# Optimization experiments

Hardware: AMD Instinct MI355X
Metric: run time of the kernel (lower is better)

The kernel has to match this reference:

```python
import jax, jax.numpy as jnp
import numpy as np

B, T, D = 8, 8192, 768

def setup_inputs() -> dict:
    key = jax.random.key(0)
    k1, k2 = jax.random.split(key)
    x = jax.random.normal(k1, (B, T, D), dtype=jnp.float32)
    stimulus = jax.random.normal(k2, (B, T, D), dtype=jnp.float32)
    return {"x": x, "stimulus": stimulus}

def reference(x, stimulus):
    # Per-position dot product: out[b, t] = sum_d x[b, t, d] * stimulus[b, t, d]
    return jnp.einsum("btd,btd->bt", x, stimulus)
```

## Files before the change

### kernel.cpp

```cpp
#include <hip/hip_runtime.h>


constexpr int D = 768;
constexpr int D4 = D / 4;
constexpr int ROWS = 8 * 8192;

__global__ __launch_bounds__(256) void row_dot_kernel(
    const float4* __restrict__ x,
    const float4* __restrict__ s,
    float* __restrict__ out)
{
    const int wave = (blockIdx.x * blockDim.x + threadIdx.x) >> 6;
    const int lane = threadIdx.x & 63;
    if (wave >= ROWS) return;

    const size_t base = (size_t)wave * D4;

    float acc = 0.0f;
#pragma unroll
    for (int c = 0; c < 3; ++c) {
        float4 a = x[base + c * 64 + lane];
        float4 b = s[base + c * 64 + lane];
        acc = fmaf(a.x, b.x, acc);
        acc = fmaf(a.y, b.y, acc);
        acc = fmaf(a.z, b.z, acc);
        acc = fmaf(a.w, b.w, acc);
    }

#pragma unroll
    for (int off = 32; off > 0; off >>= 1)
        acc += __shfl_down(acc, off, 64);

    if (lane == 0) out[wave] = acc;
}

extern "C" void kernel_launch(void* const* d_in, const int* in_sizes, int n_in,
                              void* d_out, int out_size, void* d_ws, size_t ws_size,
                              hipStream_t stream)
{
    const float4* x = (const float4*)d_in[0];
    const float4* s = (const float4*)d_in[1];
    float* out = (float*)d_out;

    const int waves_per_block = 4;
    const int blocks = ROWS / waves_per_block;
    row_dot_kernel<<<blocks, 256, 0, stream>>>(x, s, out);
}
```

Baseline: 380.9 us.

## Process eight rows per wavefront with batched loads and vectorized output stores

Each wavefront now handles eight consecutive rows instead of one, issuing all six float4 loads per row in an unrolled loop so many memory requests are in flight per wave. Reductions use xor shuffles, and lane 0 writes the eight results as two float4 stores. The grid shrinks eightfold and the launch bounds request higher occupancy. This costs more registers per thread and fewer waves overall, which could reduce latency hiding on a purely bandwidth-bound workload.

```diff
diff --git a/kernel.cpp b/kernel.cpp
--- a/kernel.cpp
+++ b/kernel.cpp
@@ -1,37 +1,61 @@
 #include <hip/hip_runtime.h>
 
 
-constexpr int D = 768;
-constexpr int D4 = D / 4;
+constexpr int D4   = 768 / 4;
 constexpr int ROWS = 8 * 8192;
+constexpr int RPW  = 8;
 
-__global__ __launch_bounds__(256) void row_dot_kernel(
+__global__ __launch_bounds__(256, 8) void row_dot_kernel(
     const float4* __restrict__ x,
     const float4* __restrict__ s,
-    float* __restrict__ out)
+    float4* __restrict__ out4)
 {
     const int wave = (blockIdx.x * blockDim.x + threadIdx.x) >> 6;
     const int lane = threadIdx.x & 63;
-    if (wave >= ROWS) return;
 
-    const size_t base = (size_t)wave * D4;
+    const size_t row0 = (size_t)wave * RPW;
 
-    float acc = 0.0f;
+    float acc[RPW];
 #pragma unroll
-    for (int c = 0; c < 3; ++c) {
-        float4 a = x[base + c * 64 + lane];
-        float4 b = s[base + c * 64 + lane];
-        acc = fmaf(a.x, b.x, acc);
-        acc = fmaf(a.y, b.y, acc);
-        acc = fmaf(a.z, b.z, acc);
-        acc = fmaf(a.w, b.w, acc);
+    for (int r = 0; r < RPW; ++r) {
+        const size_t base = (row0 + r) * D4 + lane;
+        float4 a0 = x[base];
+        float4 b0 = s[base];
+        float4 a1 = x[base + 64];
+        float4 b1 = s[base + 64];
+        float4 a2 = x[base + 128];
+        float4 b2 = s[base + 128];
+        float t = 0.0f;
+        t = fmaf(a0.x, b0.x, t);
+        t = fmaf(a0.y, b0.y, t);
+        t = fmaf(a0.z, b0.z, t);
+        t = fmaf(a0.w, b0.w, t);
+        t = fmaf(a1.x, b1.x, t);
+        t = fmaf(a1.y, b1.y, t);
+        t = fmaf(a1.z, b1.z, t);
+        t = fmaf(a1.w, b1.w, t);
+        t = fmaf(a2.x, b2.x, t);
+        t = fmaf(a2.y, b2.y, t);
+        t = fmaf(a2.z, b2.z, t);
+        t = fmaf(a2.w, b2.w, t);
+        acc[r] = t;
     }
 
 #pragma unroll
-    for (int off = 32; off > 0; off >>= 1)
-        acc += __shfl_down(acc, off, 64);
+    for (int r = 0; r < RPW; ++r) {
+        float v = acc[r];
+#pragma unroll
+        for (int off = 32; off > 0; off >>= 1)
+            v += __shfl_xor(v, off, 64);
+        acc[r] = v;
+    }
 
-    if (lane == 0) out[wave] = acc;
+    if (lane == 0) {
+        float4 o0 = make_float4(acc[0], acc[1], acc[2], acc[3]);
+        float4 o1 = make_float4(acc[4], acc[5], acc[6], acc[7]);
+        out4[(size_t)wave * 2]     = o0;
+        out4[(size_t)wave * 2 + 1] = o1;
+    }
 }
 
 extern "C" void kernel_launch(void* const* d_in, const int* in_sizes, int n_in,
@@ -40,9 +64,8 @@
 {
     const float4* x = (const float4*)d_in[0];
     const float4* s = (const float4*)d_in[1];
-    float* out = (float*)d_out;
+    float4* out4 = (float4*)d_out;
 
-    const int waves_per_block = 4;
-    const int blocks = ROWS / waves_per_block;
-    row_dot_kernel<<<blocks, 256, 0, stream>>>(x, s, out);
+    const int blocks = (ROWS / RPW) / 4;
+    row_dot_kernel<<<blocks, 256, 0, stream>>>(x, s, out4);
 }
```

Measured after the change: 388.0 us. No clear change (+1.9%).

## Process eight rows per wave with register double-buffered prefetch

Applied to the files above, without the earlier changes.

Each wavefront now handles eight consecutive rows instead of one, loading the next row's x and stimulus float4 chunks into registers while the current row is reduced. The grid shrinks eightfold and launch bounds request higher occupancy. The aim is to keep more memory requests in flight per wave and amortize launch and reduction overhead on a bandwidth-bound kernel. The cost is doubled register use for the prefetch buffers and fewer total waves to hide latency.

```diff
diff --git a/kernel.cpp b/kernel.cpp
--- a/kernel.cpp
+++ b/kernel.cpp
@@ -1,37 +1,59 @@
 #include <hip/hip_runtime.h>
 
 
-constexpr int D = 768;
-constexpr int D4 = D / 4;
+constexpr int D4   = 768 / 4;
 constexpr int ROWS = 8 * 8192;
+constexpr int RPW  = 8;
 
-__global__ __launch_bounds__(256) void row_dot_kernel(
+__global__ __launch_bounds__(256, 8) void row_dot_kernel(
     const float4* __restrict__ x,
     const float4* __restrict__ s,
     float* __restrict__ out)
 {
     const int wave = (blockIdx.x * blockDim.x + threadIdx.x) >> 6;
     const int lane = threadIdx.x & 63;
-    if (wave >= ROWS) return;
 
-    const size_t base = (size_t)wave * D4;
+    const size_t row0 = (size_t)wave * RPW;
+    size_t p = row0 * D4 + lane;
 
-    float acc = 0.0f;
-#pragma unroll
-    for (int c = 0; c < 3; ++c) {
-        float4 a = x[base + c * 64 + lane];
-        float4 b = s[base + c * 64 + lane];
-        acc = fmaf(a.x, b.x, acc);
-        acc = fmaf(a.y, b.y, acc);
-        acc = fmaf(a.z, b.z, acc);
-        acc = fmaf(a.w, b.w, acc);
-    }
+    float4 ca0 = x[p];       float4 cb0 = s[p];
+    float4 ca1 = x[p + 64];  float4 cb1 = s[p + 64];
+    float4 ca2 = x[p + 128]; float4 cb2 = s[p + 128];
 
 #pragma unroll
-    for (int off = 32; off > 0; off >>= 1)
-        acc += __shfl_down(acc, off, 64);
+    for (int r = 0; r < RPW; ++r) {
+        float4 na0, na1, na2, nb0, nb1, nb2;
+        if (r < RPW - 1) {
+            const size_t q = p + D4;
+            na0 = x[q];       nb0 = s[q];
+            na1 = x[q + 64];  nb1 = s[q + 64];
+            na2 = x[q + 128]; nb2 = s[q + 128];
+        }
 
-    if (lane == 0) out[wave] = acc;
+        float t = 0.0f;
+        t = fmaf(ca0.x, cb0.x, t);
+        t = fmaf(ca0.y, cb0.y, t);
+        t = fmaf(ca0.z, cb0.z, t);
+        t = fmaf(ca0.w, cb0.w, t);
+        t = fmaf(ca1.x, cb1.x, t);
+        t = fmaf(ca1.y, cb1.y, t);
+        t = fmaf(ca1.z, cb1.z, t);
+        t = fmaf(ca1.w, cb1.w, t);
+        t = fmaf(ca2.x, cb2.x, t);
+        t = fmaf(ca2.y, cb2.y, t);
+        t = fmaf(ca2.z, cb2.z, t);
+        t = fmaf(ca2.w, cb2.w, t);
+
+#pragma unroll
+        for (int off = 32; off > 0; off >>= 1)
+            t += __shfl_xor(t, off, 64);
+
+        if (lane == 0) out[row0 + r] = t;
+
+        p += D4;
+        ca0 = na0; ca1 = na1; ca2 = na2;
+        cb0 = nb0; cb1 = nb1; cb2 = nb2;
+    }
 }
 
 extern "C" void kernel_launch(void* const* d_in, const int* in_sizes, int n_in,
@@ -42,7 +64,6 @@
     const float4* s = (const float4*)d_in[1];
     float* out = (float*)d_out;
 
-    const int waves_per_block = 4;
-    const int blocks = ROWS / waves_per_block;
+    const int blocks = (ROWS / RPW) / 4;
     row_dot_kernel<<<blocks, 256, 0, stream>>>(x, s, out);
 }
```

After: 392.8 us. 1.03x slower.

## Process eight rows per wave with double-buffered register prefetch

Applied to the files above, without the earlier changes.

Each wave now handles eight rows, two at a time, issuing loads for the next pair before computing the current pair so more memory requests stay in flight. Reductions use xor shuffles for two rows at once, and sched_barrier keeps the compiler from reordering loads and math. This trades more registers and fewer total waves for higher per-wave memory-level parallelism and less launch and tail overhead.

```diff
diff --git a/kernel.cpp b/kernel.cpp
--- a/kernel.cpp
+++ b/kernel.cpp
@@ -1,37 +1,78 @@
 #include <hip/hip_runtime.h>
 
 
-constexpr int D = 768;
-constexpr int D4 = D / 4;
+constexpr int D4   = 768 / 4;
 constexpr int ROWS = 8 * 8192;
+constexpr int RPW  = 8;
 
-__global__ __launch_bounds__(256) void row_dot_kernel(
+__global__ __launch_bounds__(256, 4) void row_dot_kernel(
     const float4* __restrict__ x,
     const float4* __restrict__ s,
     float* __restrict__ out)
 {
     const int wave = (blockIdx.x * blockDim.x + threadIdx.x) >> 6;
     const int lane = threadIdx.x & 63;
-    if (wave >= ROWS) return;
+    const size_t row0 = (size_t)wave * RPW;
 
-    const size_t base = (size_t)wave * D4;
+    float4 ca[6], cb[6];
+    float4 na[6], nb[6];
 
-    float acc = 0.0f;
-#pragma unroll
-    for (int c = 0; c < 3; ++c) {
-        float4 a = x[base + c * 64 + lane];
-        float4 b = s[base + c * 64 + lane];
-        acc = fmaf(a.x, b.x, acc);
-        acc = fmaf(a.y, b.y, acc);
-        acc = fmaf(a.z, b.z, acc);
-        acc = fmaf(a.w, b.w, acc);
-    }
+    size_t base = row0 * D4 + lane;
 
 #pragma unroll
-    for (int off = 32; off > 0; off >>= 1)
-        acc += __shfl_down(acc, off, 64);
+    for (int j = 0; j < 2; ++j)
+#pragma unroll
+        for (int c = 0; c < 3; ++c) {
+            ca[j * 3 + c] = x[base + j * D4 + c * 64];
+            cb[j * 3 + c] = s[base + j * D4 + c * 64];
+        }
+    __builtin_amdgcn_sched_barrier(0);
 
-    if (lane == 0) out[wave] = acc;
+#pragma unroll
+    for (int p = 0; p < RPW / 2; ++p) {
+        if (p < RPW / 2 - 1) {
+            const size_t nxt = base + 2 * D4;
+#pragma unroll
+            for (int j = 0; j < 2; ++j)
+#pragma unroll
+                for (int c = 0; c < 3; ++c) {
+                    na[j * 3 + c] = x[nxt + j * D4 + c * 64];
+                    nb[j * 3 + c] = s[nxt + j * D4 + c * 64];
+                }
+        }
+        __builtin_amdgcn_sched_barrier(0);
+
+        float t0 = 0.0f, t1 = 0.0f;
+#pragma unroll
+        for (int c = 0; c < 3; ++c) {
+            t0 = fmaf(ca[c].x, cb[c].x, t0);
+            t0 = fmaf(ca[c].y, cb[c].y, t0);
+            t0 = fmaf(ca[c].z, cb[c].z, t0);
+            t0 = fmaf(ca[c].w, cb[c].w, t0);
+            t1 = fmaf(ca[3 + c].x, cb[3 + c].x, t1);
+            t1 = fmaf(ca[3 + c].y, cb[3 + c].y, t1);
+            t1 = fmaf(ca[3 + c].z, cb[3 + c].z, t1);
+            t1 = fmaf(ca[3 + c].w, cb[3 + c].w, t1);
+        }
+
+#pragma unroll
+        for (int off = 32; off > 0; off >>= 1) {
+            t0 += __shfl_xor(t0, off, 64);
+            t1 += __shfl_xor(t1, off, 64);
+        }
+
+        if (lane == 0) {
+            out[row0 + 2 * p]     = t0;
+            out[row0 + 2 * p + 1] = t1;
+        }
+
+        base += 2 * D4;
+#pragma unroll
+        for (int i = 0; i < 6; ++i) {
+            ca[i] = na[i]; cb[i] = nb[i];
+        }
+        __builtin_amdgcn_sched_barrier(0);
+    }
 }
 
 extern "C" void kernel_launch(void* const* d_in, const int* in_sizes, int n_in,
@@ -42,7 +83,6 @@
     const float4* s = (const float4*)d_in[1];
     float* out = (float*)d_out;
 
-    const int waves_per_block = 4;
-    const int blocks = ROWS / waves_per_block;
+    const int blocks = (ROWS / RPW) / 4;
     row_dot_kernel<<<blocks, 256, 0, stream>>>(x, s, out);
 }
```

Result: no change. 385.4 us (+1.2%).
